# Performance work log

Hardware: AMD Instinct MI355X
Metric: run time of the kernel (lower is better)

The kernel has to match this reference:

```python
import jax, jax.numpy as jnp
import numpy as np
import math

L = 7          # spherical-harmonic truncation -> lsize = (L+1)^2 = 64
T = 128        # number of channels/fragments in clms


def _cg_coef(j1, m1, j2, m2, j, m):
    """Clebsch-Gordan coefficient <j1 m1 j2 m2 | j m> via the Racah formula."""
    if m1 + m2 != m or not (abs(j1 - j2) <= j <= j1 + j2):
        return 0.0
    f = math.factorial
    pref = math.sqrt((2 * j + 1) * f(j1 + j2 - j) * f(j1 - j2 + j)
                     * f(-j1 + j2 + j) / f(j1 + j2 + j + 1))
    pref *= math.sqrt(f(j + m) * f(j - m) * f(j1 - m1) * f(j1 + m1)
                      * f(j2 - m2) * f(j2 + m2))
    kmin = max(0, j2 - j - m1, j1 + m2 - j)
    kmax = min(j1 + j2 - j, j1 - m1, j2 + m2)
    s = 0.0
    for k in range(kmin, kmax + 1):
        s += (-1) ** k / (f(k) * f(j1 + j2 - j - k) * f(j1 - m1 - k)
                          * f(j2 + m2 - k) * f(j - j2 + m1 + k) * f(j - j1 - m2 + k))
    return pref * s


def _idx(l, m):
    return l * l + l + m


def _build_C(L):
    """Dense packed CG tensor C[(l,m),(l1,m1),(l2,m2)], zero outside selection rules."""
    lsize = (L + 1) ** 2
    C = np.zeros((lsize, lsize, lsize), dtype=np.float64)
    for l1 in range(L + 1):
        for l2 in range(L + 1):
            for l in range(abs(l1 - l2), min(l1 + l2, L) + 1):
                for m1 in range(-l1, l1 + 1):
                    for m2 in range(-l2, l2 + 1):
                        m = m1 + m2
                        if abs(m) <= l:
                            C[_idx(l, m), _idx(l1, m1), _idx(l2, m2)] = \
                                _cg_coef(l1, m1, l2, m2, l, m)
    return C.astype(np.float32)


def setup_inputs() -> dict:
    key = jax.random.key(0)
    clms = jax.random.normal(key, ((L + 1) ** 2, T), dtype=jnp.float32)
    C = jnp.asarray(_build_C(L))
    return {"clms": clms, "C": C}


def reference(clms, C):
    lsize = clms.shape[0]
    Lc = int(math.isqrt(lsize)) - 1
    Tn = clms.shape[1]
    # full Kronecker product, blockwise indexed by (l1,m1),(l2,m2); [lsize, lsize, T^2]
    Gs = (clms[:, None, :, None] * clms[None, :, None, :]).reshape(lsize, lsize, Tn * Tn)
    temp = [[] for _ in range(Lc + 1)]
    for l1 in range(Lc + 1):
        for l2 in range(Lc + 1):
            g = Gs[l1 * l1:(l1 + 1) ** 2, l2 * l2:(l2 + 1) ** 2, :]
            cg = C[:, l1 * l1:(l1 + 1) ** 2, l2 * l2:(l2 + 1) ** 2]
            # cg @ g over the flattened (m1,m2) block -> [(Lc+1)^2, T^2]
            prod = jnp.einsum('kij,ijt->kt', cg, g)
            for l in range(abs(l1 - l2), min(l1 + l2, Lc) + 1):
                temp[l].append(prod[l * l:(l + 1) ** 2, :])
    return tuple(jnp.concatenate(t, axis=1) for t in temp)
```

## Files before the change

kernel.cpp:

```cpp
#include <hip/hip_runtime.h>

#define TDIM 128

__host__ __device__ inline int trivalid(int l, int l1, int l2) {
  int d = l1 - l2; if (d < 0) d = -d;
  return (l >= d && l <= l1 + l2) ? 1 : 0;
}

__device__ __forceinline__ float u2f(unsigned int u) {
  union { unsigned int u; float f; } w; w.u = u; return w.f;
}
__device__ __forceinline__ float bf2f(unsigned short v) {
  return u2f(((unsigned int)v) << 16);
}
__device__ __forceinline__ unsigned short f2bf(float x) {
  union { float f; unsigned int u; } w; w.f = x;
  unsigned int u = w.u;
  u += 0x7fffu + ((u >> 16) & 1u);
  return (unsigned short)(u >> 16);
}

__global__ __launch_bounds__(256, 4)
void cg_kernel(const void* __restrict__ clms_raw,
               const void* __restrict__ C_raw,
               void* __restrict__ out_raw) {
  __shared__ float sc[64 * TDIM];
  __shared__ float scoef[16];

  const int tid = threadIdx.x;

  const unsigned int* cw = (const unsigned int*)clms_raw;
  int cnt_bf = 0;
  #pragma unroll
  for (int i = 0; i < 32; ++i) {
    unsigned int e = (cw[i] >> 7) & 0xFFu;
    cnt_bf += (e >= 110u && e <= 135u) ? 1 : 0;
  }
  const bool in_bf16 = (cnt_bf >= 16);
  const bool c_bf16 = ((*(const unsigned int*)C_raw) & 0xffffu) == 0x3f80u;

  if (tid < 16) scoef[tid] = 0.0f;

  if (in_bf16) {
    const uint4* cl4 = (const uint4*)clms_raw;
    #pragma unroll
    for (int it = 0; it < 4; ++it) {
      int v = tid + it * 256;
      uint4 w = cl4[v];
      float4* dst = (float4*)&sc[v * 8];
      float4 d0, d1;
      d0.x = u2f(w.x << 16); d0.y = u2f(w.x & 0xffff0000u);
      d0.z = u2f(w.y << 16); d0.w = u2f(w.y & 0xffff0000u);
      d1.x = u2f(w.z << 16); d1.y = u2f(w.z & 0xffff0000u);
      d1.z = u2f(w.w << 16); d1.w = u2f(w.w & 0xffff0000u);
      dst[0] = d0; dst[1] = d1;
    }
  } else {
    const float4* cf4 = (const float4*)clms_raw;
    float4* sc4 = (float4*)sc;
    #pragma unroll
    for (int it = 0; it < 8; ++it) {
      int v = tid + it * 256;
      sc4[v] = cf4[v];
    }
  }

  const int r = blockIdx.x;
  int rem = r, l = 0, cnt = 0;
  for (l = 0; l < 8; ++l) {
    cnt = 0;
    for (int a = 0; a < 8; ++a)
      for (int b = 0; b < 8; ++b) cnt += trivalid(l, a, b);
    int rows = (2 * l + 1) * cnt;
    if (rem < rows) break;
    rem -= rows;
  }
  const int mi = rem / cnt;
  const int p  = rem - mi * cnt;
  const int m  = mi - l;
  int l1 = 0, l2 = 0;
  {
    int q = 0; bool done = false;
    for (int a = 0; a < 8 && !done; ++a)
      for (int b = 0; b < 8; ++b) {
        if (trivalid(l, a, b)) {
          if (q == p) { l1 = a; l2 = b; done = true; break; }
          ++q;
        }
      }
  }

  int m1lo = (-l1 > m - l2) ? -l1 : (m - l2);
  int m1hi = ( l1 < m + l2) ?  l1 : (m + l2);
  const int nnz = m1hi - m1lo + 1;

  if (tid < nnz) {
    int m1 = m1lo + tid;
    int m2 = m - m1;
    int i  = l1 * (l1 + 1) + m1;
    int j  = l2 * (l2 + 1) + m2;
    int k  = l  * (l  + 1) + m;
    int ci = ((k * 64) + i) * 64 + j;
    scoef[tid] = c_bf16 ? bf2f(((const unsigned short*)C_raw)[ci])
                        : ((const float*)C_raw)[ci];
  }
  __syncthreads();

  float creg[15];
  #pragma unroll
  for (int q = 0; q < 15; ++q) creg[q] = scoef[q];

  const int tx = tid & 31;
  const int ty = tid >> 5;
  const int t2 = tx * 4;
  const int i0 = l1 * (l1 + 1) + m1lo;
  const int j0 = l2 * (l2 + 1) + m - m1lo;

  int arow[15], brow[15];
  #pragma unroll
  for (int q = 0; q < 15; ++q) {
    int qc = (q < nnz) ? q : 0;
    arow[q] = (i0 + qc) * TDIM;
    brow[q] = (j0 - qc) * TDIM;
  }

  float4 b[15];
  #pragma unroll
  for (int q = 0; q < 15; ++q) b[q] = *(const float4*)&sc[brow[q] + t2];

  const unsigned long long outbase = (unsigned long long)r * (TDIM * TDIM);

  if (in_bf16) {
    unsigned short* out = (unsigned short*)out_raw;
    #pragma unroll 4
    for (int s = 0; s < 16; ++s) {
      const int t1 = ty + 8 * s;
      float4 acc = make_float4(0.f, 0.f, 0.f, 0.f);
      #pragma unroll
      for (int q = 0; q < 15; ++q) {
        if (q < nnz) {
          float ca = creg[q] * sc[arow[q] + t1];
          acc.x += ca * b[q].x;  acc.y += ca * b[q].y;
          acc.z += ca * b[q].z;  acc.w += ca * b[q].w;
        }
      }
      ushort4 o;
      o.x = f2bf(acc.x); o.y = f2bf(acc.y);
      o.z = f2bf(acc.z); o.w = f2bf(acc.w);
      *(ushort4*)(out + outbase + (unsigned long long)(t1 * TDIM + t2)) = o;
    }
  } else {
    float* out = (float*)out_raw;
    #pragma unroll 4
    for (int s = 0; s < 16; ++s) {
      const int t1 = ty + 8 * s;
      float4 acc = make_float4(0.f, 0.f, 0.f, 0.f);
      #pragma unroll
      for (int q = 0; q < 15; ++q) {
        if (q < nnz) {
          float ca = creg[q] * sc[arow[q] + t1];
          acc.x += ca * b[q].x;  acc.y += ca * b[q].y;
          acc.z += ca * b[q].z;  acc.w += ca * b[q].w;
        }
      }
      *(float4*)(out + outbase + (unsigned long long)(t1 * TDIM + t2)) = acc;
    }
  }
}

extern "C" void kernel_launch(void* const* d_in, const int* in_sizes, int n_in,
                              void* d_out, int out_size, void* d_ws, size_t ws_size,
                              hipStream_t stream) {
  (void)in_sizes; (void)n_in; (void)d_ws; (void)ws_size;
  const int nrows = out_size / (TDIM * TDIM);
  cg_kernel<<<nrows, 256, 0, stream>>>(d_in[0], d_in[1], d_out);
}
```

Before: 173.4 us.

## Compute per-row outer product with bf16 MFMA instead of scalar FMAs

For bf16 inputs, stages coefficient-scaled A rows and B rows into LDS as K-padded bf16 tiles and computes each 128x128 output block with 16x16x32 bf16 MFMA instructions. This replaces the scalar FMA loop over up to 15 terms. The fp32 path drops the LDS staging and reads clms straight from global memory. The change trades scalar compute for matrix-core work, at the cost of padding K to 32, narrower per-element output stores, and an extra bf16 rounding of the coefficient-scaled A values.

Result: slower. 193.0 us (+11.3%).

```diff
diff --git a/kernel.cpp b/kernel.cpp
--- a/kernel.cpp
+++ b/kernel.cpp
@@ -1,6 +1,10 @@
 #include <hip/hip_runtime.h>
 
 #define TDIM 128
+#define KP 40
+
+typedef __attribute__((ext_vector_type(8))) short short8;
+typedef __attribute__((ext_vector_type(4))) float float4v;
 
 __host__ __device__ inline int trivalid(int l, int l1, int l2) {
   int d = l1 - l2; if (d < 0) d = -d;
@@ -20,12 +24,13 @@
   return (unsigned short)(u >> 16);
 }
 
-__global__ __launch_bounds__(256, 4)
+__global__ __launch_bounds__(256)
 void cg_kernel(const void* __restrict__ clms_raw,
                const void* __restrict__ C_raw,
                void* __restrict__ out_raw) {
-  __shared__ float sc[64 * TDIM];
-  __shared__ float scoef[16];
+  __shared__ unsigned short sa[TDIM * KP];
+  __shared__ unsigned short sb[TDIM * KP];
+  __shared__ float scoef[32];
 
   const int tid = threadIdx.x;
 
@@ -38,32 +43,6 @@
   }
   const bool in_bf16 = (cnt_bf >= 16);
   const bool c_bf16 = ((*(const unsigned int*)C_raw) & 0xffffu) == 0x3f80u;
-
-  if (tid < 16) scoef[tid] = 0.0f;
-
-  if (in_bf16) {
-    const uint4* cl4 = (const uint4*)clms_raw;
-    #pragma unroll
-    for (int it = 0; it < 4; ++it) {
-      int v = tid + it * 256;
-      uint4 w = cl4[v];
-      float4* dst = (float4*)&sc[v * 8];
-      float4 d0, d1;
-      d0.x = u2f(w.x << 16); d0.y = u2f(w.x & 0xffff0000u);
-      d0.z = u2f(w.y << 16); d0.w = u2f(w.y & 0xffff0000u);
-      d1.x = u2f(w.z << 16); d1.y = u2f(w.z & 0xffff0000u);
-      d1.z = u2f(w.w << 16); d1.w = u2f(w.w & 0xffff0000u);
-      dst[0] = d0; dst[1] = d1;
-    }
-  } else {
-    const float4* cf4 = (const float4*)clms_raw;
-    float4* sc4 = (float4*)sc;
-    #pragma unroll
-    for (int it = 0; it < 8; ++it) {
-      int v = tid + it * 256;
-      sc4[v] = cf4[v];
-    }
-  }
 
   const int r = blockIdx.x;
   int rem = r, l = 0, cnt = 0;
@@ -90,80 +69,92 @@
       }
   }
 
-  int m1lo = (-l1 > m - l2) ? -l1 : (m - l2);
-  int m1hi = ( l1 < m + l2) ?  l1 : (m + l2);
+  const int m1lo = (-l1 > m - l2) ? -l1 : (m - l2);
+  const int m1hi = ( l1 < m + l2) ?  l1 : (m + l2);
   const int nnz = m1hi - m1lo + 1;
+  const int i0 = l1 * (l1 + 1) + m1lo;
+  const int j0 = l2 * (l2 + 1) + m - m1lo;
 
-  if (tid < nnz) {
-    int m1 = m1lo + tid;
-    int m2 = m - m1;
-    int i  = l1 * (l1 + 1) + m1;
-    int j  = l2 * (l2 + 1) + m2;
-    int k  = l  * (l  + 1) + m;
-    int ci = ((k * 64) + i) * 64 + j;
-    scoef[tid] = c_bf16 ? bf2f(((const unsigned short*)C_raw)[ci])
-                        : ((const float*)C_raw)[ci];
+  if (tid < 32) {
+    float v = 0.0f;
+    if (tid < nnz) {
+      int m1 = m1lo + tid, m2 = m - m1;
+      int i = l1 * (l1 + 1) + m1;
+      int j = l2 * (l2 + 1) + m2;
+      int k = l  * (l  + 1) + m;
+      int ci = (k * 64 + i) * 64 + j;
+      v = c_bf16 ? bf2f(((const unsigned short*)C_raw)[ci])
+                 : ((const float*)C_raw)[ci];
+    }
+    scoef[tid] = v;
   }
   __syncthreads();
 
-  float creg[15];
-  #pragma unroll
-  for (int q = 0; q < 15; ++q) creg[q] = scoef[q];
+  if (in_bf16) {
+    const unsigned short* cl = (const unsigned short*)clms_raw;
+    #pragma unroll
+    for (int c0 = 0; c0 < 2; ++c0) {
+      int c  = tid + c0 * 256;
+      int t  = c >> 2;
+      int kc = c & 3;
+      union { unsigned short u[8]; uint4 v; } pa, pb;
+      #pragma unroll
+      for (int j = 0; j < 8; ++j) {
+        int k  = kc * 8 + j;
+        int qa = (k < nnz) ? k : 0;
+        unsigned short araw = cl[(i0 + qa) * TDIM + t];
+        unsigned short braw = cl[(j0 - qa) * TDIM + t];
+        pa.u[j] = (k < nnz) ? f2bf(scoef[k] * bf2f(araw)) : (unsigned short)0;
+        pb.u[j] = (k < nnz) ? braw : (unsigned short)0;
+      }
+      *(uint4*)&sa[t * KP + kc * 8] = pa.v;
+      *(uint4*)&sb[t * KP + kc * 8] = pb.v;
+    }
+    __syncthreads();
 
-  const int tx = tid & 31;
-  const int ty = tid >> 5;
-  const int t2 = tx * 4;
-  const int i0 = l1 * (l1 + 1) + m1lo;
-  const int j0 = l2 * (l2 + 1) + m - m1lo;
+    const int lane = tid & 63;
+    const int w    = tid >> 6;
+    const int col  = lane & 15;
+    const int quad = lane >> 4;
+    unsigned short* outp = (unsigned short*)out_raw;
+    const unsigned long long outbase = (unsigned long long)r * (TDIM * TDIM);
 
-  int arow[15], brow[15];
-  #pragma unroll
-  for (int q = 0; q < 15; ++q) {
-    int qc = (q < nnz) ? q : 0;
-    arow[q] = (i0 + qc) * TDIM;
-    brow[q] = (j0 - qc) * TDIM;
-  }
+    short8 af0 = *(const short8*)&sa[((2 * w + 0) * 16 + col) * KP + quad * 8];
+    short8 af1 = *(const short8*)&sa[((2 * w + 1) * 16 + col) * KP + quad * 8];
 
-  float4 b[15];
-  #pragma unroll
-  for (int q = 0; q < 15; ++q) b[q] = *(const float4*)&sc[brow[q] + t2];
-
-  const unsigned long long outbase = (unsigned long long)r * (TDIM * TDIM);
-
-  if (in_bf16) {
-    unsigned short* out = (unsigned short*)out_raw;
-    #pragma unroll 4
-    for (int s = 0; s < 16; ++s) {
-      const int t1 = ty + 8 * s;
-      float4 acc = make_float4(0.f, 0.f, 0.f, 0.f);
+    #pragma unroll
+    for (int tn = 0; tn < 8; ++tn) {
+      short8 bf = *(const short8*)&sb[(tn * 16 + col) * KP + quad * 8];
+      float4v acc0 = {0.f, 0.f, 0.f, 0.f};
+      float4v acc1 = {0.f, 0.f, 0.f, 0.f};
+      acc0 = __builtin_amdgcn_mfma_f32_16x16x32_bf16(af0, bf, acc0, 0, 0, 0);
+      acc1 = __builtin_amdgcn_mfma_f32_16x16x32_bf16(af1, bf, acc1, 0, 0, 0);
       #pragma unroll
-      for (int q = 0; q < 15; ++q) {
-        if (q < nnz) {
-          float ca = creg[q] * sc[arow[q] + t1];
-          acc.x += ca * b[q].x;  acc.y += ca * b[q].y;
-          acc.z += ca * b[q].z;  acc.w += ca * b[q].w;
-        }
+      for (int rg = 0; rg < 4; ++rg) {
+        int t1a = (2 * w + 0) * 16 + quad * 4 + rg;
+        int t1b = (2 * w + 1) * 16 + quad * 4 + rg;
+        outp[outbase + (unsigned long long)(t1a * TDIM + tn * 16 + col)] = f2bf(acc0[rg]);
+        outp[outbase + (unsigned long long)(t1b * TDIM + tn * 16 + col)] = f2bf(acc1[rg]);
       }
-      ushort4 o;
-      o.x = f2bf(acc.x); o.y = f2bf(acc.y);
-      o.z = f2bf(acc.z); o.w = f2bf(acc.w);
-      *(ushort4*)(out + outbase + (unsigned long long)(t1 * TDIM + t2)) = o;
     }
   } else {
-    float* out = (float*)out_raw;
-    #pragma unroll 4
+    __syncthreads();
+    const float* clf = (const float*)clms_raw;
+    float* outp = (float*)out_raw;
+    const int tx = tid & 31;
+    const int ty = tid >> 5;
+    const int t2 = tx * 4;
+    const unsigned long long outbase = (unsigned long long)r * (TDIM * TDIM);
     for (int s = 0; s < 16; ++s) {
-      const int t1 = ty + 8 * s;
-      float4 acc = make_float4(0.f, 0.f, 0.f, 0.f);
-      #pragma unroll
-      for (int q = 0; q < 15; ++q) {
-        if (q < nnz) {
-          float ca = creg[q] * sc[arow[q] + t1];
-          acc.x += ca * b[q].x;  acc.y += ca * b[q].y;
-          acc.z += ca * b[q].z;  acc.w += ca * b[q].w;
-        }
+      int t1 = ty + 8 * s;
+      float ax = 0.f, ay = 0.f, az = 0.f, aw = 0.f;
+      for (int q = 0; q < nnz; ++q) {
+        float ca = scoef[q] * clf[(i0 + q) * TDIM + t1];
+        const float* bp = &clf[(j0 - q) * TDIM + t2];
+        ax += ca * bp[0]; ay += ca * bp[1]; az += ca * bp[2]; aw += ca * bp[3];
       }
-      *(float4*)(out + outbase + (unsigned long long)(t1 * TDIM + t2)) = acc;
+      float4 o; o.x = ax; o.y = ay; o.z = az; o.w = aw;
+      *(float4*)(outp + outbase + (unsigned long long)(t1 * TDIM + t2)) = o;
     }
   }
 }
```
